# Optimization experiments

Measured on AMD Instinct MI355X. Metric: run time of the kernel, lower is better.

Reference implementation:

```python
import jax, jax.numpy as jnp
import numpy as np
import math

D_MODEL = 1024
D_STATE = 16
D_CONV = 4
EXPAND = 2
D_INNER = EXPAND * D_MODEL
DT_RANK = max(D_MODEL // 16, 1)
B_SZ, L_SEQ = 2, 2048
DT_MIN, DT_MAX = 1e-3, 1e-1


def setup_inputs() -> dict:
    key = jax.random.key(0)
    ks = jax.random.split(key, 10)
    x = jax.random.normal(ks[0], (B_SZ, L_SEQ, D_MODEL), dtype=jnp.float32)
    # torch nn.Linear weights are [out, in]
    in_proj_w = jax.random.normal(ks[1], (2 * D_INNER, D_MODEL), jnp.float32) * 0.02
    conv_w = jax.random.normal(ks[2], (D_INNER, 1, D_CONV), jnp.float32) * 0.2  # depthwise [d,1,k]
    conv_b = jax.random.normal(ks[3], (D_INNER,), jnp.float32) * 0.02
    x_proj_w = jax.random.normal(ks[4], (DT_RANK + 2 * D_STATE, D_INNER), jnp.float32) * 0.02
    dt_init_std = DT_RANK ** -0.5
    dt_proj_w = jax.random.uniform(ks[5], (D_INNER, DT_RANK), jnp.float32, -dt_init_std, dt_init_std)
    dt = jnp.exp(jax.random.uniform(ks[6], (D_INNER,)) * (math.log(DT_MAX) - math.log(DT_MIN)) + math.log(DT_MIN))
    dt = jnp.clip(dt, DT_MIN, None)
    dt_proj_b = dt + jnp.log(-jnp.expm1(-dt))  # inverse softplus
    A = jnp.tile(jnp.arange(1, D_STATE + 1, dtype=jnp.float32)[None, :], (D_INNER, 1))
    A_log = jnp.log(A)
    D_param = jnp.ones((D_INNER,), jnp.float32)
    out_proj_w = jax.random.normal(ks[7], (D_MODEL, D_INNER), jnp.float32) * 0.02
    return {"x": x, "in_proj_w": in_proj_w, "conv_w": conv_w, "conv_b": conv_b,
            "x_proj_w": x_proj_w, "dt_proj_w": dt_proj_w, "dt_proj_b": dt_proj_b,
            "A_log": A_log, "D_param": D_param, "out_proj_w": out_proj_w}


def _ssm_forward(x, in_proj_w, conv_w, conv_b, x_proj_w, dt_proj_w, dt_proj_b, A_log, D_param, out_proj_w):
    B, L, _ = x.shape
    xz = jnp.einsum('bld,ed->ble', x, in_proj_w)          # [B,L,2*d_inner]
    x_branch, z = jnp.split(xz, 2, axis=-1)               # each [B,L,d_inner]
    # causal depthwise conv over L
    xc = jnp.transpose(x_branch, (0, 2, 1))               # [B,d,L]
    xc = jnp.pad(xc, ((0, 0), (0, 0), (D_CONV - 1, 0)))
    xc = jax.lax.conv_general_dilated(xc, conv_w, window_strides=(1,), padding='VALID',
                                      feature_group_count=D_INNER)
    xc = xc + conv_b[None, :, None]
    x_conv = jax.nn.silu(jnp.transpose(xc, (0, 2, 1)))    # [B,L,d_inner]
    # input-dependent projections
    xp = jnp.einsum('bld,ed->ble', x_conv, x_proj_w)      # [B,L,dt_rank+2n]
    dt_low, Bp, Cp = jnp.split(xp, [DT_RANK, DT_RANK + D_STATE], axis=-1)
    dt = jax.nn.softplus(jnp.einsum('blr,dr->bld', dt_low, dt_proj_w) + dt_proj_b)  # [B,L,d]
    A = -jnp.exp(A_log)                                   # [d,n]
    # sequential selective scan via lax.scan (time-major inputs)
    def step(h, inp):
        dt_t, B_t, C_t, x_t = inp                         # [B,d],[B,n],[B,n],[B,d]
        dA = jnp.exp(dt_t[:, :, None] * A[None])          # [B,d,n]
        h = dA * h + (dt_t * x_t)[:, :, None] * B_t[:, None, :]
        y = jnp.einsum('bdn,bn->bd', h, C_t)
        return h, y

    h0 = jnp.zeros((B, D_INNER, D_STATE), x.dtype)
    xs = (jnp.swapaxes(dt, 0, 1), jnp.swapaxes(Bp, 0, 1), jnp.swapaxes(Cp, 0, 1), jnp.swapaxes(x_conv, 0, 1))
    _, ys = jax.lax.scan(step, h0, xs)                    # ys: [L,B,d]
    y = jnp.swapaxes(ys, 0, 1)                            # [B,L,d]
    y = y + D_param * x_conv
    y = y * jax.nn.silu(z)
    return jnp.einsum('bld,ed->ble', y, out_proj_w)       # [B,L,d_model]


def reference(x, in_proj_w, conv_w, conv_b, x_proj_w, dt_proj_w, dt_proj_b, A_log, D_param, out_proj_w):
    return _ssm_forward(x, in_proj_w, conv_w, conv_b, x_proj_w, dt_proj_w, dt_proj_b, A_log, D_param, out_proj_w)
```

## Files before the change

kernel.cpp:

```cpp
#include <hip/hip_runtime.h>
#include <math.h>

#define BB      2
#define LSEQ    2048
#define DMODEL  1024
#define DINNER  2048
#define DSTATE  16
#define DTRANK  64
#define NPROJ   96
#define MROWS   (BB * LSEQ)
#define NCHUNK  64
#define CLEN    32
#define XKS     16

typedef unsigned short u16;
typedef short bf16x8 __attribute__((ext_vector_type(8)));
typedef float f32x4  __attribute__((ext_vector_type(4)));

struct HL { unsigned int hx, hy, lx, ly; };

__device__ __forceinline__ HL cvt4(float4 v) {
  unsigned int tx = __float_as_uint(v.x) & 0xFFFF0000u;
  unsigned int ty = __float_as_uint(v.y) & 0xFFFF0000u;
  unsigned int tz = __float_as_uint(v.z) & 0xFFFF0000u;
  unsigned int tw = __float_as_uint(v.w) & 0xFFFF0000u;
  HL r;
  r.hx = (tx >> 16) | ty;
  r.hy = (tz >> 16) | tw;
  float lx = v.x - __uint_as_float(tx);
  float ly = v.y - __uint_as_float(ty);
  float lz = v.z - __uint_as_float(tz);
  float lw = v.w - __uint_as_float(tw);
  unsigned int a = __float_as_uint(lx); a += 0x7FFFu + ((a >> 16) & 1u);
  unsigned int b = __float_as_uint(ly); b += 0x7FFFu + ((b >> 16) & 1u);
  unsigned int c = __float_as_uint(lz); c += 0x7FFFu + ((c >> 16) & 1u);
  unsigned int d = __float_as_uint(lw); d += 0x7FFFu + ((d >> 16) & 1u);
  r.lx = (a >> 16) | (b & 0xFFFF0000u);
  r.ly = (c >> 16) | (d & 0xFFFF0000u);
  return r;
}

__global__ __launch_bounds__(256)
void cvt_hl(const float4* __restrict__ src, uint2* __restrict__ dh,
            uint2* __restrict__ dl, int n4) {
  int i = blockIdx.x * 256 + threadIdx.x;
  if (i < n4) {
    HL r = cvt4(src[i]);
    dh[i] = make_uint2(r.hx, r.hy);
    dl[i] = make_uint2(r.lx, r.ly);
  }
}

__device__ __forceinline__ void gll16(const void* g, void* l) {
  __builtin_amdgcn_global_load_lds(
      (const __attribute__((address_space(1))) void*)g,
      (__attribute__((address_space(3))) void*)l, 16, 0, 0);
}

__global__ __launch_bounds__(256, 3)
void gemm_hl(const u16* __restrict__ Ahp, const u16* __restrict__ Alp,
             const u16* __restrict__ Bhp, const u16* __restrict__ Blp,
             float* __restrict__ C0, float* __restrict__ C1,
             int M, int N, int K, int Nout, int XC_C) {
  __shared__ __align__(16) u16 L[4][128 * 32];

  const int tid = threadIdx.x;
  const int nbx = N >> 7, nby = M >> 7;
  const int xcd = blockIdx.x & 7;
  const int pos = blockIdx.x >> 3;
  const int cr = xcd / XC_C, cc = xcd - cr * XC_C;
  const int GCc = nbx / XC_C;
  const int GR  = (nby * XC_C) >> 3;
  const int by = cr * GR + pos / GCc;
  const int bx = cc * GCc + pos % GCc;
  const int row0 = by << 7, col0 = bx << 7;

  const int lane = tid & 63, w = tid >> 6;
  const int wr = w >> 1, wc = w & 1;
  const int fr = lane & 15, g = lane >> 4;
  const int lrow = lane >> 2, lslot = lane & 3;

  f32x4 acc[4][4] = {};

  for (int k0 = 0; k0 < K; k0 += 32) {
#pragma unroll
    for (int s = 0; s < 2; ++s) {
      const int r = w * 32 + s * 16 + lrow;
      const int csrc = (lslot ^ ((r >> 1) & 3)) << 3;
      const size_t gA = (size_t)(row0 + r) * K + k0 + csrc;
      const size_t gB = (size_t)(col0 + r) * K + k0 + csrc;
      const int lb = w * 1024 + s * 512;
      gll16(Ahp + gA, &L[0][lb]);
      gll16(Alp + gA, &L[1][lb]);
      gll16(Bhp + gB, &L[2][lb]);
      gll16(Blp + gB, &L[3][lb]);
    }
    __syncthreads();

    bf16x8 bh[4], bl[4];
#pragma unroll
    for (int j = 0; j < 4; ++j) {
      const int rb = wc * 64 + j * 16 + fr;
      const int o = rb * 32 + ((g ^ ((rb >> 1) & 3)) << 3);
      bh[j] = *(const bf16x8*)&L[2][o];
      bl[j] = *(const bf16x8*)&L[3][o];
    }
#pragma unroll
    for (int i = 0; i < 4; ++i) {
      const int ra = wr * 64 + i * 16 + fr;
      const int o = ra * 32 + ((g ^ ((ra >> 1) & 3)) << 3);
      bf16x8 ah = *(const bf16x8*)&L[0][o];
      bf16x8 al = *(const bf16x8*)&L[1][o];
#pragma unroll
      for (int j = 0; j < 4; ++j) {
        acc[i][j] = __builtin_amdgcn_mfma_f32_16x16x32_bf16(al, bh[j], acc[i][j], 0, 0, 0);
        acc[i][j] = __builtin_amdgcn_mfma_f32_16x16x32_bf16(ah, bl[j], acc[i][j], 0, 0, 0);
        acc[i][j] = __builtin_amdgcn_mfma_f32_16x16x32_bf16(ah, bh[j], acc[i][j], 0, 0, 0);
      }
    }
    __syncthreads();
  }

  float* Cd;
  int cc0;
  if (C1 != nullptr && col0 >= Nout) { Cd = C1; cc0 = col0 - Nout; }
  else                               { Cd = C0; cc0 = col0; }
#pragma unroll
  for (int i = 0; i < 4; ++i) {
    const int rbase = row0 + wr * 64 + i * 16 + (lane >> 4) * 4;
#pragma unroll
    for (int j = 0; j < 4; ++j) {
      const int cfull = cc0 + wc * 64 + j * 16 + fr;
#pragma unroll
      for (int r = 0; r < 4; ++r)
        Cd[(size_t)(rbase + r) * Nout + cfull] = acc[i][j][r];
    }
  }
}

template <int ACT>
__global__ __launch_bounds__(256)
void gemm_tn(const float* __restrict__ A, const float* __restrict__ B,
             float* __restrict__ C, const float* __restrict__ bias,
             int M, int N, int K, int lda) {
  __shared__ float As[8][128];
  __shared__ float Bs[8][128];
  const int tid  = threadIdx.x;
  const int row0 = blockIdx.y * 128;
  const int col0 = blockIdx.x * 128;
  const int tx = tid & 15, ty = tid >> 4;
  const int lr = tid >> 1;
  const int lk = (tid & 1) * 4;

  float acc[8][8];
#pragma unroll
  for (int i = 0; i < 8; ++i)
#pragma unroll
    for (int j = 0; j < 8; ++j) acc[i][j] = 0.f;

  const float* Aptr = A + (size_t)(row0 + lr) * lda + lk;
  const int bcol = col0 + lr;
  const float* Bptr = (bcol < N) ? (B + (size_t)bcol * K + lk) : nullptr;

  float4 av = *(const float4*)(Aptr);
  float4 bv = Bptr ? *(const float4*)(Bptr) : make_float4(0.f, 0.f, 0.f, 0.f);

  for (int k0 = 0; k0 < K; k0 += 8) {
    As[lk + 0][lr] = av.x; As[lk + 1][lr] = av.y;
    As[lk + 2][lr] = av.z; As[lk + 3][lr] = av.w;
    Bs[lk + 0][lr] = bv.x; Bs[lk + 1][lr] = bv.y;
    Bs[lk + 2][lr] = bv.z; Bs[lk + 3][lr] = bv.w;
    if (k0 + 8 < K) {
      av = *(const float4*)(Aptr + k0 + 8);
      if (Bptr) bv = *(const float4*)(Bptr + k0 + 8);
    }
    __syncthreads();
#pragma unroll
    for (int k = 0; k < 8; ++k) {
      float a[8], b[8];
      *(float4*)&a[0] = *(const float4*)&As[k][ty * 4];
      *(float4*)&a[4] = *(const float4*)&As[k][64 + ty * 4];
      *(float4*)&b[0] = *(const float4*)&Bs[k][tx * 4];
      *(float4*)&b[4] = *(const float4*)&Bs[k][64 + tx * 4];
#pragma unroll
      for (int i = 0; i < 8; ++i)
#pragma unroll
        for (int j = 0; j < 8; ++j)
          acc[i][j] = fmaf(a[i], b[j], acc[i][j]);
    }
    __syncthreads();
  }

#pragma unroll
  for (int ih = 0; ih < 2; ++ih) {
#pragma unroll
    for (int i2 = 0; i2 < 4; ++i2) {
      int r = row0 + ih * 64 + ty * 4 + i2;
      if (r >= M) continue;
#pragma unroll
      for (int jh = 0; jh < 2; ++jh) {
        int c = col0 + jh * 64 + tx * 4;
        float vv[4];
#pragma unroll
        for (int j = 0; j < 4; ++j) {
          float v = acc[ih * 4 + i2][jh * 4 + j];
          if (ACT == 1) {
            v += bias[c + j];
            v = (v > 20.f) ? v : log1pf(expf(v));
          }
          vv[j] = v;
        }
        if (c + 3 < N) {
          *(float4*)(C + (size_t)r * N + c) = make_float4(vv[0], vv[1], vv[2], vv[3]);
        } else {
          for (int j = 0; j < 4; ++j)
            if (c + j < N) C[(size_t)r * N + c + j] = vv[j];
        }
      }
    }
  }
}

__global__ __launch_bounds__(256)
void xproj_splitk(const float* __restrict__ A, const float* __restrict__ W,
                  float* __restrict__ Pq) {
  __shared__ float As[8][128];
  __shared__ float Ws[8][96];
  const int tid  = threadIdx.x;
  const int row0 = blockIdx.x * 128;
  const int k0b  = blockIdx.y * (DINNER / XKS);
  const int tx = tid & 15, ty = tid >> 4;
  const int lr = tid >> 1, lk = (tid & 1) * 4;

  float acc[8][6];
#pragma unroll
  for (int i = 0; i < 8; ++i)
#pragma unroll
    for (int j = 0; j < 6; ++j) acc[i][j] = 0.f;

  const float* Ap = A + (size_t)(row0 + lr) * DINNER + lk;
  const float* Wp = (tid < 192) ? (W + (size_t)(tid >> 1) * DINNER + (tid & 1) * 4)
                                : nullptr;
  float4 av = *(const float4*)(Ap + k0b);
  float4 wv = Wp ? *(const float4*)(Wp + k0b) : make_float4(0.f, 0.f, 0.f, 0.f);

  for (int k0 = k0b; k0 < k0b + DINNER / XKS; k0 += 8) {
    As[lk + 0][lr] = av.x; As[lk + 1][lr] = av.y;
    As[lk + 2][lr] = av.z; As[lk + 3][lr] = av.w;
    if (Wp) {
      int j = tid >> 1, kk = (tid & 1) * 4;
      Ws[kk + 0][j] = wv.x; Ws[kk + 1][j] = wv.y;
      Ws[kk + 2][j] = wv.z; Ws[kk + 3][j] = wv.w;
    }
    if (k0 + 8 < k0b + DINNER / XKS) {
      av = *(const float4*)(Ap + k0 + 8);
      if (Wp) wv = *(const float4*)(Wp + k0 + 8);
    }
    __syncthreads();
#pragma unroll
    for (int kk = 0; kk < 8; ++kk) {
      float a[8], w[6];
      *(float4*)&a[0] = *(const float4*)&As[kk][ty * 8];
      *(float4*)&a[4] = *(const float4*)&As[kk][ty * 8 + 4];
#pragma unroll
      for (int j = 0; j < 6; ++j) w[j] = Ws[kk][tx * 6 + j];
#pragma unroll
      for (int i = 0; i < 8; ++i)
#pragma unroll
        for (int j = 0; j < 6; ++j)
          acc[i][j] = fmaf(a[i], w[j], acc[i][j]);
    }
    __syncthreads();
  }
  float* dst = Pq + (size_t)blockIdx.y * (MROWS * NPROJ);
#pragma unroll
  for (int i = 0; i < 8; ++i)
#pragma unroll
    for (int j = 0; j < 6; ++j)
      dst[(size_t)(row0 + ty * 8 + i) * NPROJ + tx * 6 + j] = acc[i][j];
}

__global__ __launch_bounds__(256)
void xpj_reduce(const float* __restrict__ Pq, float* __restrict__ xpb) {
  int idx = blockIdx.x * 256 + threadIdx.x;
  float s = 0.f;
#pragma unroll
  for (int q = 0; q < XKS; ++q)
    s += Pq[(size_t)q * (MROWS * NPROJ) + idx];
  xpb[idx] = s;
}

__global__ __launch_bounds__(256)
void conv_silu_kernel(const float* __restrict__ xb, const float* __restrict__ cw,
                      const float* __restrict__ cb, float* __restrict__ xc) {
  int idx = (blockIdx.x * 256 + threadIdx.x) * 4;
  int d  = idx & (DINNER - 1);
  int ml = idx >> 11;
  int l  = ml & (LSEQ - 1);
  float4 W0 = *(const float4*)(cw + (d + 0) * 4);
  float4 W1 = *(const float4*)(cw + (d + 1) * 4);
  float4 W2 = *(const float4*)(cw + (d + 2) * 4);
  float4 W3 = *(const float4*)(cw + (d + 3) * 4);
  const float* base = xb + (size_t)ml * DINNER + d;
  float4 z4 = make_float4(0.f, 0.f, 0.f, 0.f);
  float4 r0  = *(const float4*)(base);
  float4 rm1 = (l >= 1) ? *(const float4*)(base - DINNER)     : z4;
  float4 rm2 = (l >= 2) ? *(const float4*)(base - 2 * DINNER) : z4;
  float4 rm3 = (l >= 3) ? *(const float4*)(base - 3 * DINNER) : z4;
  float4 bias = *(const float4*)(cb + d);
  float4 o;
  o.x = bias.x + r0.x * W0.w + rm1.x * W0.z + rm2.x * W0.y + rm3.x * W0.x;
  o.y = bias.y + r0.y * W1.w + rm1.y * W1.z + rm2.y * W1.y + rm3.y * W1.x;
  o.z = bias.z + r0.z * W2.w + rm1.z * W2.z + rm2.z * W2.y + rm3.z * W2.x;
  o.w = bias.w + r0.w * W3.w + rm1.w * W3.z + rm2.w * W3.y + rm3.w * W3.x;
  o.x = o.x / (1.f + expf(-o.x));
  o.y = o.y / (1.f + expf(-o.y));
  o.z = o.z / (1.f + expf(-o.z));
  o.w = o.w / (1.f + expf(-o.w));
  *(float4*)(xc + idx) = o;
}

__global__ __launch_bounds__(256)
void scan_chunk_kernel(const float* __restrict__ dt, const float* __restrict__ xp,
                       const float* __restrict__ xc, const float* __restrict__ A_log,
                       float* __restrict__ P, float* __restrict__ H) {
  __shared__ float sbc[CLEN][32];
  const int tid = threadIdx.x;
  const int bid = blockIdx.x;
  const int b  = bid >> 9;
  const int c  = (bid >> 3) & 63;
  const int dg = bid & 7;
  const int d  = dg * 256 + tid;
  const int m0 = b * LSEQ + c * CLEN;
  {
    int r = tid >> 3, q = (tid & 7) * 4;
    *(float4*)&sbc[r][q] = *(const float4*)(xp + (size_t)(m0 + r) * NPROJ + DTRANK + q);
  }
  float a2[DSTATE], h[DSTATE];
#pragma unroll
  for (int n = 0; n < DSTATE; ++n) {
    a2[n] = -expf(A_log[d * DSTATE + n]) * 1.44269504f;
    h[n] = 0.f;
  }
  float dtsum = 0.f;
  __syncthreads();

  const float* dtp = dt + (size_t)m0 * DINNER + d;
  const float* xcp = xc + (size_t)m0 * DINNER + d;
  float ndt = dtp[0], nxc = xcp[0];
  for (int s = 0; s < CLEN; ++s) {
    float dtv = ndt, xv = nxc;
    int sp = (s + 1 < CLEN) ? s + 1 : s;
    ndt = dtp[(size_t)sp * DINNER];
    nxc = xcp[(size_t)sp * DINNER];
    dtsum += dtv;
    float dtx = dtv * xv;
    float Bv[16];
    *(float4*)&Bv[0]  = *(const float4*)&sbc[s][0];
    *(float4*)&Bv[4]  = *(const float4*)&sbc[s][4];
    *(float4*)&Bv[8]  = *(const float4*)&sbc[s][8];
    *(float4*)&Bv[12] = *(const float4*)&sbc[s][12];
#pragma unroll
    for (int n = 0; n < DSTATE; ++n) {
      float a = exp2f(dtv * a2[n]);
      h[n] = fmaf(a, h[n], dtx * Bv[n]);
    }
  }
  size_t o = ((size_t)(b * NCHUNK + c) * DINNER + d) * DSTATE;
  float4* Hp = (float4*)(H + o);
  Hp[0] = make_float4(h[0], h[1], h[2], h[3]);
  Hp[1] = make_float4(h[4], h[5], h[6], h[7]);
  Hp[2] = make_float4(h[8], h[9], h[10], h[11]);
  Hp[3] = make_float4(h[12], h[13], h[14], h[15]);
  float p[16];
#pragma unroll
  for (int n = 0; n < DSTATE; ++n) p[n] = exp2f(a2[n] * dtsum);
  float4* Pp = (float4*)(P + o);
  Pp[0] = make_float4(p[0], p[1], p[2], p[3]);
  Pp[1] = make_float4(p[4], p[5], p[6], p[7]);
  Pp[2] = make_float4(p[8], p[9], p[10], p[11]);
  Pp[3] = make_float4(p[12], p[13], p[14], p[15]);
}

__global__ __launch_bounds__(256)
void stitch_kernel(const float* __restrict__ P, float* __restrict__ H) {
  int idx = blockIdx.x * 256 + threadIdx.x;
  int b = idx >> 15, e = idx & 32767;
  size_t base = (size_t)b * NCHUNK * 32768 + e;
  float h = 0.f;
  for (int c = 0; c < NCHUNK; ++c) {
    size_t o = base + (size_t)c * 32768;
    float p = P[o], q = H[o];
    H[o] = h;
    h = fmaf(p, h, q);
  }
}

__global__ __launch_bounds__(256)
void scan_out_kernel(const float* dt, const float* __restrict__ xp,
                     const float* __restrict__ xc, const float* __restrict__ z,
                     const float* __restrict__ A_log, const float* __restrict__ Dp,
                     const float* __restrict__ Hinit, float* y) {
  __shared__ float sbc[CLEN][32];
  const int tid = threadIdx.x;
  const int bid = blockIdx.x;
  const int b  = bid >> 9;
  const int c  = (bid >> 3) & 63;
  const int dg = bid & 7;
  const int d  = dg * 256 + tid;
  const int m0 = b * LSEQ + c * CLEN;
  {
    int r = tid >> 3, q = (tid & 7) * 4;
    *(float4*)&sbc[r][q] = *(const float4*)(xp + (size_t)(m0 + r) * NPROJ + DTRANK + q);
  }
  float a2[DSTATE], h[DSTATE];
  size_t ho = ((size_t)(b * NCHUNK + c) * DINNER + d) * DSTATE;
  const float4* Hp = (const float4*)(Hinit + ho);
  float4 h0 = Hp[0], h1 = Hp[1], h2 = Hp[2], h3 = Hp[3];
  h[0]=h0.x; h[1]=h0.y; h[2]=h0.z; h[3]=h0.w;
  h[4]=h1.x; h[5]=h1.y; h[6]=h1.z; h[7]=h1.w;
  h[8]=h2.x; h[9]=h2.y; h[10]=h2.z; h[11]=h2.w;
  h[12]=h3.x; h[13]=h3.y; h[14]=h3.z; h[15]=h3.w;
#pragma unroll
  for (int n = 0; n < DSTATE; ++n)
    a2[n] = -expf(A_log[d * DSTATE + n]) * 1.44269504f;
  const float Dv = Dp[d];
  __syncthreads();

  const float* dtp = dt + (size_t)m0 * DINNER + d;
  const float* xcp = xc + (size_t)m0 * DINNER + d;
  const float* zp  = z  + (size_t)m0 * DINNER + d;
  float* yp = y + (size_t)m0 * DINNER + d;
  float ndt = dtp[0], nxc = xcp[0], nz = zp[0];
  for (int s = 0; s < CLEN; ++s) {
    float dtv = ndt, xv = nxc, zv = nz;
    int sp = (s + 1 < CLEN) ? s + 1 : s;
    ndt = dtp[(size_t)sp * DINNER];
    nxc = xcp[(size_t)sp * DINNER];
    nz  = zp[(size_t)sp * DINNER];
    float dtx = dtv * xv;
    float Bv[16], Cv[16];
    *(float4*)&Bv[0]  = *(const float4*)&sbc[s][0];
    *(float4*)&Bv[4]  = *(const float4*)&sbc[s][4];
    *(float4*)&Bv[8]  = *(const float4*)&sbc[s][8];
    *(float4*)&Bv[12] = *(const float4*)&sbc[s][12];
    *(float4*)&Cv[0]  = *(const float4*)&sbc[s][16];
    *(float4*)&Cv[4]  = *(const float4*)&sbc[s][20];
    *(float4*)&Cv[8]  = *(const float4*)&sbc[s][24];
    *(float4*)&Cv[12] = *(const float4*)&sbc[s][28];
    float yv = 0.f;
#pragma unroll
    for (int n = 0; n < DSTATE; ++n) {
      float a = exp2f(dtv * a2[n]);
      h[n] = fmaf(a, h[n], dtx * Bv[n]);
      yv = fmaf(h[n], Cv[n], yv);
    }
    yv = (yv + Dv * xv) * (zv / (1.f + expf(-zv)));
    yp[(size_t)s * DINNER] = yv;
  }
}

extern "C" void kernel_launch(void* const* d_in, const int* in_sizes, int n_in,
                              void* d_out, int out_size, void* d_ws, size_t ws_size,
                              hipStream_t stream) {
  const float* x          = (const float*)d_in[0];
  const float* in_proj_w  = (const float*)d_in[1];
  const float* conv_w     = (const float*)d_in[2];
  const float* conv_b     = (const float*)d_in[3];
  const float* x_proj_w   = (const float*)d_in[4];
  const float* dt_proj_w  = (const float*)d_in[5];
  const float* dt_proj_b  = (const float*)d_in[6];
  const float* A_log      = (const float*)d_in[7];
  const float* D_param    = (const float*)d_in[8];
  const float* out_proj_w = (const float*)d_in[9];
  float* out = (float*)d_out;
  float* ws  = (float*)d_ws;

  float* xb   = ws;
  float* dtr  = xb;
  float* zb   = ws + 8388608;
  float* xcb  = ws + 16777216;
  float* xpb  = ws + 25165824;
  float* Pbuf = ws + 25559040;
  float* Hbuf = ws + 29753344;
  float* Pq   = Pbuf;

  u16* xh = (u16*)(ws + 16777216);
  u16* xl = (u16*)(ws + 16777216 + 2097152);
  u16* wh = (u16*)(ws + 16777216 + 4194304);
  u16* wl = (u16*)(ws + 16777216 + 6291456);
  u16* yh = (u16*)(ws + 16777216);
  u16* yl = (u16*)(ws + 16777216 + 4194304);
  u16* oh = (u16*)(ws + 25559040);
  u16* ol = (u16*)(ws + 25559040 + 1048576);

  dim3 blk(256);
  cvt_hl<<<4096, blk, 0, stream>>>((const float4*)x, (uint2*)xh, (uint2*)xl, 1048576);
  cvt_hl<<<4096, blk, 0, stream>>>((const float4*)in_proj_w, (uint2*)wh, (uint2*)wl, 1048576);
  gemm_hl<<<dim3((MROWS / 128) * (2 * DINNER / 128)), blk, 0, stream>>>(
      xh, xl, wh, wl, xb, zb, MROWS, 2 * DINNER, DMODEL, DINNER, 4);
  conv_silu_kernel<<<(MROWS * DINNER) / 1024, blk, 0, stream>>>(xb, conv_w, conv_b, xcb);
  xproj_splitk<<<dim3(MROWS / 128, XKS), blk, 0, stream>>>(xcb, x_proj_w, Pq);
  xpj_reduce<<<(MROWS * NPROJ) / 256, blk, 0, stream>>>(Pq, xpb);
  gemm_tn<1><<<dim3(DINNER / 128, MROWS / 128), blk, 0, stream>>>(
      xpb, dt_proj_w, dtr, dt_proj_b, MROWS, DINNER, DTRANK, NPROJ);
  scan_chunk_kernel<<<dim3(BB * NCHUNK * 8), blk, 0, stream>>>(
      dtr, xpb, xcb, A_log, Pbuf, Hbuf);
  stitch_kernel<<<dim3(BB * DINNER * DSTATE / 256), blk, 0, stream>>>(Pbuf, Hbuf);
  scan_out_kernel<<<dim3(BB * NCHUNK * 8), blk, 0, stream>>>(
      dtr, xpb, xcb, zb, A_log, D_param, Hbuf, xb);
  cvt_hl<<<8192, blk, 0, stream>>>((const float4*)xb, (uint2*)yh, (uint2*)yl, 2097152);
  cvt_hl<<<2048, blk, 0, stream>>>((const float4*)out_proj_w, (uint2*)oh, (uint2*)ol, 524288);
  gemm_hl<<<dim3((MROWS / 128) * (DMODEL / 128)), blk, 0, stream>>>(
      yh, yl, oh, ol, out, out, MROWS, DMODEL, DINNER, DMODEL, 1);
}
```

Measured before the change: 521.4 us.

## Use 256x256 tile double-buffered GEMM kernel for in_proj

```diff
diff --git a/kernel.cpp b/kernel.cpp
--- a/kernel.cpp
+++ b/kernel.cpp
@@ -55,6 +55,103 @@
   __builtin_amdgcn_global_load_lds(
       (const __attribute__((address_space(1))) void*)g,
       (__attribute__((address_space(3))) void*)l, 16, 0, 0);
+}
+
+__global__ __launch_bounds__(512, 1)
+void gemm_hl256(const u16* __restrict__ Ahp, const u16* __restrict__ Alp,
+                const u16* __restrict__ Bhp, const u16* __restrict__ Blp,
+                float* __restrict__ C0, float* __restrict__ C1,
+                int M, int N, int K, int Nout, int XC_C) {
+  __shared__ __align__(16) u16 L[2][4][256 * 32];
+
+  const int tid = threadIdx.x;
+  const int nbx = N >> 8, nby = M >> 8;
+  const int xcd = blockIdx.x & 7;
+  const int pos = blockIdx.x >> 3;
+  const int cr = xcd / XC_C, cc = xcd - cr * XC_C;
+  const int GCc = nbx / XC_C;
+  const int GR  = (nby * XC_C) >> 3;
+  const int by = cr * GR + pos / GCc;
+  const int bx = cc * GCc + pos % GCc;
+  const int row0 = by << 8, col0 = bx << 8;
+
+  const int lane = tid & 63, w = tid >> 6;
+  const int wr = w >> 2, wc = w & 3;
+  const int fr = lane & 15, g = lane >> 4;
+  const int lrow = lane >> 2, lslot = lane & 3;
+
+  f32x4 acc[8][4] = {};
+  const int NT = K >> 5;
+
+#define STAGE256(pb, k0)                                                   \
+  {                                                                        \
+    _Pragma("unroll")                                                      \
+    for (int s = 0; s < 2; ++s) {                                          \
+      const int r = w * 32 + s * 16 + lrow;                                \
+      const int csrc = (lslot ^ ((r >> 1) & 3)) << 3;                      \
+      const size_t gA = (size_t)(row0 + r) * K + (k0) + csrc;              \
+      const size_t gB = (size_t)(col0 + r) * K + (k0) + csrc;              \
+      const int lb = w * 1024 + s * 512;                                   \
+      gll16(Ahp + gA, &L[pb][0][lb]);                                      \
+      gll16(Alp + gA, &L[pb][1][lb]);                                      \
+      gll16(Bhp + gB, &L[pb][2][lb]);                                      \
+      gll16(Blp + gB, &L[pb][3][lb]);                                      \
+    }                                                                      \
+  }
+
+  STAGE256(0, 0);
+  asm volatile("s_waitcnt vmcnt(0)" ::: "memory");
+  __syncthreads();
+
+  int p = 0;
+  for (int t = 0; t < NT; ++t) {
+    const bool pf = (t + 1 < NT);
+    if (pf) STAGE256(p ^ 1, (t + 1) * 32);
+
+    bf16x8 bh[4], bl[4];
+#pragma unroll
+    for (int j = 0; j < 4; ++j) {
+      const int rb = wc * 64 + j * 16 + fr;
+      const int o = rb * 32 + ((g ^ ((rb >> 1) & 3)) << 3);
+      bh[j] = *(const bf16x8*)&L[p][2][o];
+      bl[j] = *(const bf16x8*)&L[p][3][o];
+    }
+#pragma unroll
+    for (int i = 0; i < 8; ++i) {
+      const int ra = wr * 128 + i * 16 + fr;
+      const int o = ra * 32 + ((g ^ ((ra >> 1) & 3)) << 3);
+      bf16x8 ah = *(const bf16x8*)&L[p][0][o];
+      bf16x8 al = *(const bf16x8*)&L[p][1][o];
+#pragma unroll
+      for (int j = 0; j < 4; ++j) {
+        acc[i][j] = __builtin_amdgcn_mfma_f32_16x16x32_bf16(al, bh[j], acc[i][j], 0, 0, 0);
+        acc[i][j] = __builtin_amdgcn_mfma_f32_16x16x32_bf16(ah, bl[j], acc[i][j], 0, 0, 0);
+        acc[i][j] = __builtin_amdgcn_mfma_f32_16x16x32_bf16(ah, bh[j], acc[i][j], 0, 0, 0);
+      }
+    }
+    if (pf) {
+      asm volatile("s_waitcnt vmcnt(0)" ::: "memory");
+      __syncthreads();
+    }
+    p ^= 1;
+  }
+
+  float* Cd;
+  int cc0;
+  if (C1 != nullptr && col0 >= Nout) { Cd = C1; cc0 = col0 - Nout; }
+  else                               { Cd = C0; cc0 = col0; }
+#pragma unroll
+  for (int i = 0; i < 8; ++i) {
+    const int rbase = row0 + wr * 128 + i * 16 + (lane >> 4) * 4;
+#pragma unroll
+    for (int j = 0; j < 4; ++j) {
+      const int cfull = cc0 + wc * 64 + j * 16 + fr;
+#pragma unroll
+      for (int r = 0; r < 4; ++r)
+        Cd[(size_t)(rbase + r) * Nout + cfull] = acc[i][j][r];
+    }
+  }
+#undef STAGE256
 }
 
 __global__ __launch_bounds__(256, 3)
@@ -497,7 +594,7 @@
   dim3 blk(256);
   cvt_hl<<<4096, blk, 0, stream>>>((const float4*)x, (uint2*)xh, (uint2*)xl, 1048576);
   cvt_hl<<<4096, blk, 0, stream>>>((const float4*)in_proj_w, (uint2*)wh, (uint2*)wl, 1048576);
-  gemm_hl<<<dim3((MROWS / 128) * (2 * DINNER / 128)), blk, 0, stream>>>(
+  gemm_hl256<<<dim3((MROWS / 256) * (2 * DINNER / 256)), dim3(512), 0, stream>>>(
       xh, xl, wh, wl, xb, zb, MROWS, 2 * DINNER, DMODEL, DINNER, 4);
   conv_silu_kernel<<<(MROWS * DINNER) / 1024, blk, 0, stream>>>(xb, conv_w, conv_b, xcb);
   xproj_splitk<<<dim3(MROWS / 128, XKS), blk, 0, stream>>>(xcb, x_proj_w, Pq);
```

Result: faster. 499.5 us (-4.2%).
